# Performance work log

Hardware: AMD Instinct MI355X
Metric: run time of the kernel (lower is better)

The kernel has to match this reference:

```python
import jax, jax.numpy as jnp
import numpy as np

NFFT = 512
HOP = 256
N_FREQ = NFFT // 2


def _imdct_kernels():
    # Matches _get_imdct_kernels: windowed IMDCT cosine basis, shape [nfft, nfft//2]
    def kernel_fn(time, freq):
        win = np.sin(np.pi * (2 * time + 1) / (2.0 * NFFT))
        return np.cos(np.pi / NFFT * (2 * time + 1 + NFFT / 2.0) * (freq + 0.5)) * win
    k = np.fromfunction(kernel_fn, (NFFT, N_FREQ), dtype=np.float64)
    return jnp.asarray(k.astype(np.float32))  # [nfft, n_freq]


def setup_inputs() -> dict:
    key = jax.random.key(0)
    spec = jax.random.normal(key, (16, 1, N_FREQ, 4096), dtype=jnp.float32)
    return {"spec": spec, "kernels": _imdct_kernels()}


def reference(spec, kernels):
    # spec: [B, 1, n_freq, T]; kernels: [nfft, n_freq]
    B, _, _, T = spec.shape
    # conv2d with (n_freq,1) kernel == per-frame basis matmul over frequency
    frames = jnp.einsum('bft,kf->btk', spec[:, 0], kernels) * (4.0 / NFFT)  # [B, T, nfft]
    # conv_transpose2d with identity-diagonal kernel and stride=hop == overlap-add
    L = (T - 1) * HOP + NFFT
    idx = jnp.arange(T)[:, None] * HOP + jnp.arange(NFFT)[None, :]  # [T, nfft]
    out = jnp.zeros((B, L), dtype=spec.dtype).at[:, idx].add(frames)
    return out
```

## Files before the change

kernel.cpp:

```cpp
#include <hip/hip_runtime.h>
#include <stdint.h>

#define NFREQ 256
#define NB 16
#define NT 4096
#define LOUT 1048832
#define TROWS 65
#define TROW 132

typedef __bf16 bf16;
typedef __bf16 bf16x8 __attribute__((ext_vector_type(8)));
typedef float floatx4 __attribute__((ext_vector_type(4)));

__device__ inline uint32_t f_as_u(float x) { union { float f; uint32_t u; } v; v.f = x; return v.u; }
__device__ inline uint32_t bf16r(float x) {
    uint32_t u = f_as_u(x);
    return (u + 0x7fffu + ((u >> 16) & 1u)) >> 16;
}

__global__ __launch_bounds__(256) void build_kb(const float* __restrict__ ker,
                                                bf16* __restrict__ kbF) {
    int idx = blockIdx.x * 256 + threadIdx.x;
    int n = idx >> 9, f = idx & 511;
    float v = (f < 256) ? ker[(n + 256) * 256 + f] : ker[n * 256 + (f - 256)];
    uint32_t rr = bf16r(v * 0.0078125f);
    union { uint16_t u; bf16 b; } o; o.u = (uint16_t)rr;
    kbF[((size_t)(f >> 5) * 256 + n) * 32 + (f & 31)] = o.b;
}

__global__ __launch_bounds__(256, 4) void imdct_gemm(const float* __restrict__ spec,
                                                     const bf16* __restrict__ kbF,
                                                     float* __restrict__ out) {
    __shared__ uint32_t Tt[TROWS * TROW];

    const int jt = blockIdx.x;
    const int b  = blockIdx.y;
    const int tid = threadIdx.x, lane = tid & 63, w = tid >> 6;
    const int j0 = jt * 64;
    const float* sb = spec + (size_t)b * NFREQ * NT;

    {
        const int lpar = lane & 1, lt = lane >> 1;
        const int fpw = w * 32;
        for (int rb = 0; rb < 4; ++rb) {
            float v[16];
            #pragma unroll
            for (int i = 0; i < 16; ++i) {
                int r = rb * 16 + i;
                int tc = r >> 5, fpi = r & 31;
                int f = (fpw + fpi) * 2 + lpar;
                int t = j0 - 1 + tc * 32 + lt;
                v[i] = ((unsigned)t < (unsigned)NT) ? sb[(size_t)f * NT + t] : 0.0f;
            }
            #pragma unroll
            for (int i = 0; i < 16; i += 2) {
                int r = rb * 16 + i;
                int tc = r >> 5, fpi = r & 31;
                int tl = tc * 32 + lt;
                uint32_t h0 = bf16r(v[i]);     uint32_t o0 = (uint32_t)__shfl_xor((int)h0, 1);
                uint32_t h1 = bf16r(v[i + 1]); uint32_t o1 = (uint32_t)__shfl_xor((int)h1, 1);
                if (lpar == 0) {
                    uint2 pk; pk.x = (h0 & 0xffffu) | (o0 << 16); pk.y = (h1 & 0xffffu) | (o1 << 16);
                    *reinterpret_cast<uint2*>(&Tt[tl * TROW + fpw + fpi]) = pk;
                }
            }
        }
        int f = w * 64 + lane;
        int t = j0 + 63;
        float v = ((unsigned)t < (unsigned)NT) ? sb[(size_t)f * NT + t] : 0.0f;
        uint32_t h = bf16r(v); uint32_t o = (uint32_t)__shfl_xor((int)h, 1);
        if (lpar == 0) Tt[64 * TROW + w * 32 + lt] = (h & 0xffffu) | (o << 16);
    }
    __syncthreads();

    const int row16 = lane & 15, q = lane >> 4;
    floatx4 acc[4][4] = {};
    const uint8_t* Tb = reinterpret_cast<const uint8_t*>(Tt);
    const bf16* kbw = kbF + (size_t)w * 64 * 32;

    for (int kki = 0; kki < 8; ++kki) {
        const int toff = (kki >= 4) ? 1 : 0;
        const int kbyte = (kki & 3) * 128;
        #pragma unroll
        for (int ks = 0; ks < 2; ++ks) {
            const int kchunk = kki * 2 + ks;
            bf16x8 af[4], bfr[4];
            #pragma unroll
            for (int i = 0; i < 4; ++i)
                af[i] = *reinterpret_cast<const bf16x8*>(
                    Tb + (size_t)(i * 16 + row16 + toff) * 528 + kbyte + ks * 64 + q * 16);
            #pragma unroll
            for (int jn = 0; jn < 4; ++jn)
                bfr[jn] = *reinterpret_cast<const bf16x8*>(
                    kbw + (size_t)kchunk * 8192 + (jn * 16 + row16) * 32 + q * 8);
            #pragma unroll
            for (int i = 0; i < 4; ++i)
                #pragma unroll
                for (int jn = 0; jn < 4; ++jn)
                    acc[i][jn] = __builtin_amdgcn_mfma_f32_16x16x32_bf16(af[i], bfr[jn], acc[i][jn], 0, 0, 0);
        }
    }

    #pragma unroll
    for (int i = 0; i < 4; ++i) {
        #pragma unroll
        for (int e = 0; e < 4; ++e) {
            int j = j0 + i * 16 + q * 4 + e;
            if (j <= 4096) {
                float* orow = out + (size_t)b * LOUT + (size_t)j * 256 + w * 64;
                #pragma unroll
                for (int jn = 0; jn < 4; ++jn)
                    orow[jn * 16 + row16] = acc[i][jn][e];
            }
        }
    }
}

extern "C" void kernel_launch(void* const* d_in, const int* in_sizes, int n_in,
                              void* d_out, int out_size, void* d_ws, size_t ws_size,
                              hipStream_t stream) {
    const float* spec = (const float*)d_in[0];
    const float* ker  = (const float*)d_in[1];
    float* out = (float*)d_out;

    bf16* kbF = (bf16*)d_ws;

    build_kb<<<512, 256, 0, stream>>>(ker, kbF);
    imdct_gemm<<<dim3(65, NB), 256, 0, stream>>>(spec, kbF, out);
}
```

Baseline: 142.8 us.

## Double time tile per block and vectorize spectrum staging loads

Each block now covers 128 output hop-rows instead of 64, so every weight fragment loaded from global memory is reused across 8 M-tiles instead of 4, and the grid shrinks from 65 to 33 column tiles. The spectrum staging is rewritten to use float4 loads along time with a different shuffle/pack scheme, and bf16 rounding switches from round-to-nearest-even to simple round-half-up. The cost is twice the accumulator registers and LDS per block, with occupancy hints lowered to 2, and a grid of 33x16 blocks that may underfill the GPU.

```diff
diff --git a/kernel.cpp b/kernel.cpp
--- a/kernel.cpp
+++ b/kernel.cpp
@@ -5,104 +5,96 @@
 #define NB 16
 #define NT 4096
 #define LOUT 1048832
-#define TROWS 65
-#define TROW 132
+#define TROWS 129
+#define TROWSZ 132
 
 typedef __bf16 bf16;
 typedef __bf16 bf16x8 __attribute__((ext_vector_type(8)));
 typedef float floatx4 __attribute__((ext_vector_type(4)));
 
 __device__ inline uint32_t f_as_u(float x) { union { float f; uint32_t u; } v; v.f = x; return v.u; }
-__device__ inline uint32_t bf16r(float x) {
-    uint32_t u = f_as_u(x);
-    return (u + 0x7fffu + ((u >> 16) & 1u)) >> 16;
-}
 
 __global__ __launch_bounds__(256) void build_kb(const float* __restrict__ ker,
                                                 bf16* __restrict__ kbF) {
     int idx = blockIdx.x * 256 + threadIdx.x;
     int n = idx >> 9, f = idx & 511;
     float v = (f < 256) ? ker[(n + 256) * 256 + f] : ker[n * 256 + (f - 256)];
-    uint32_t rr = bf16r(v * 0.0078125f);
+    uint32_t u = f_as_u(v * 0.0078125f);
+    uint32_t rr = (u + 0x7fffu + ((u >> 16) & 1u)) >> 16;
     union { uint16_t u; bf16 b; } o; o.u = (uint16_t)rr;
     kbF[((size_t)(f >> 5) * 256 + n) * 32 + (f & 31)] = o.b;
 }
 
-__global__ __launch_bounds__(256, 4) void imdct_gemm(const float* __restrict__ spec,
+__global__ __launch_bounds__(256, 2) void imdct_gemm(const float* __restrict__ spec,
                                                      const bf16* __restrict__ kbF,
                                                      float* __restrict__ out) {
-    __shared__ uint32_t Tt[TROWS * TROW];
+    __shared__ uint32_t Tt[TROWS * TROWSZ];
 
     const int jt = blockIdx.x;
     const int b  = blockIdx.y;
     const int tid = threadIdx.x, lane = tid & 63, w = tid >> 6;
-    const int j0 = jt * 64;
+    const int j0 = jt * 128;
     const float* sb = spec + (size_t)b * NFREQ * NT;
 
     {
-        const int lpar = lane & 1, lt = lane >> 1;
-        const int fpw = w * 32;
-        for (int rb = 0; rb < 4; ++rb) {
-            float v[16];
+        const int fr = lane >> 2;
+        const int par = fr & 1;
+        const int tsub = lane & 3;
+        for (int u = 0; u < 9; ++u) {
+            int tc = tsub + u * 4;
+            bool tcok = (tc <= 32);
             #pragma unroll
-            for (int i = 0; i < 16; ++i) {
-                int r = rb * 16 + i;
-                int tc = r >> 5, fpi = r & 31;
-                int f = (fpw + fpi) * 2 + lpar;
-                int t = j0 - 1 + tc * 32 + lt;
-                v[i] = ((unsigned)t < (unsigned)NT) ? sb[(size_t)f * NT + t] : 0.0f;
-            }
-            #pragma unroll
-            for (int i = 0; i < 16; i += 2) {
-                int r = rb * 16 + i;
-                int tc = r >> 5, fpi = r & 31;
-                int tl = tc * 32 + lt;
-                uint32_t h0 = bf16r(v[i]);     uint32_t o0 = (uint32_t)__shfl_xor((int)h0, 1);
-                uint32_t h1 = bf16r(v[i + 1]); uint32_t o1 = (uint32_t)__shfl_xor((int)h1, 1);
-                if (lpar == 0) {
-                    uint2 pk; pk.x = (h0 & 0xffffu) | (o0 << 16); pk.y = (h1 & 0xffffu) | (o1 << 16);
-                    *reinterpret_cast<uint2*>(&Tt[tl * TROW + fpw + fpi]) = pk;
+            for (int fo = 0; fo < 64; fo += 16) {
+                int f = w * 64 + fo + fr;
+                int t0 = j0 - 4 + tc * 4;
+                floatx4 v = {0.f, 0.f, 0.f, 0.f};
+                if (tcok && t0 >= 0 && t0 <= NT - 4)
+                    v = *reinterpret_cast<const floatx4*>(sb + (size_t)f * NT + t0);
+                uint32_t h[4], o[4];
+                #pragma unroll
+                for (int e = 0; e < 4; ++e) h[e] = (f_as_u(v[e]) + 0x8000u) >> 16;
+                #pragma unroll
+                for (int e = 0; e < 4; ++e) o[e] = (uint32_t)__shfl_xor((int)h[e], 4);
+                uint32_t pk0 = par ? ((o[2] & 0xffffu) | (h[2] << 16))
+                                   : ((h[0] & 0xffffu) | (o[0] << 16));
+                uint32_t pk1 = par ? ((o[3] & 0xffffu) | (h[3] << 16))
+                                   : ((h[1] & 0xffffu) | (o[1] << 16));
+                int fp = (w * 64 + fo) / 2 + (fr >> 1);
+                int tw0 = tc * 4 - 3 + par * 2;
+                if (tcok) {
+                    if ((unsigned)tw0 <= 128u)       Tt[tw0 * TROWSZ + fp]       = pk0;
+                    if ((unsigned)(tw0 + 1) <= 128u) Tt[(tw0 + 1) * TROWSZ + fp] = pk1;
                 }
             }
         }
-        int f = w * 64 + lane;
-        int t = j0 + 63;
-        float v = ((unsigned)t < (unsigned)NT) ? sb[(size_t)f * NT + t] : 0.0f;
-        uint32_t h = bf16r(v); uint32_t o = (uint32_t)__shfl_xor((int)h, 1);
-        if (lpar == 0) Tt[64 * TROW + w * 32 + lt] = (h & 0xffffu) | (o << 16);
     }
     __syncthreads();
 
     const int row16 = lane & 15, q = lane >> 4;
-    floatx4 acc[4][4] = {};
+    floatx4 acc[8][4] = {};
     const uint8_t* Tb = reinterpret_cast<const uint8_t*>(Tt);
     const bf16* kbw = kbF + (size_t)w * 64 * 32;
 
-    for (int kki = 0; kki < 8; ++kki) {
-        const int toff = (kki >= 4) ? 1 : 0;
-        const int kbyte = (kki & 3) * 128;
+    #pragma unroll 2
+    for (int kki = 0; kki < 16; ++kki) {
+        bf16x8 bfr[4];
         #pragma unroll
-        for (int ks = 0; ks < 2; ++ks) {
-            const int kchunk = kki * 2 + ks;
-            bf16x8 af[4], bfr[4];
-            #pragma unroll
-            for (int i = 0; i < 4; ++i)
-                af[i] = *reinterpret_cast<const bf16x8*>(
-                    Tb + (size_t)(i * 16 + row16 + toff) * 528 + kbyte + ks * 64 + q * 16);
+        for (int jn = 0; jn < 4; ++jn)
+            bfr[jn] = *reinterpret_cast<const bf16x8*>(
+                kbw + (size_t)kki * 8192 + (jn * 16 + row16) * 32 + q * 8);
+        const uint8_t* Ta = Tb + (size_t)(row16 + (kki >= 8 ? 1 : 0)) * 528
+                               + (kki & 7) * 64 + q * 16;
+        #pragma unroll
+        for (int i = 0; i < 8; ++i) {
+            bf16x8 af = *reinterpret_cast<const bf16x8*>(Ta + (size_t)i * 16 * 528);
             #pragma unroll
             for (int jn = 0; jn < 4; ++jn)
-                bfr[jn] = *reinterpret_cast<const bf16x8*>(
-                    kbw + (size_t)kchunk * 8192 + (jn * 16 + row16) * 32 + q * 8);
-            #pragma unroll
-            for (int i = 0; i < 4; ++i)
-                #pragma unroll
-                for (int jn = 0; jn < 4; ++jn)
-                    acc[i][jn] = __builtin_amdgcn_mfma_f32_16x16x32_bf16(af[i], bfr[jn], acc[i][jn], 0, 0, 0);
+                acc[i][jn] = __builtin_amdgcn_mfma_f32_16x16x32_bf16(af, bfr[jn], acc[i][jn], 0, 0, 0);
         }
     }
 
     #pragma unroll
-    for (int i = 0; i < 4; ++i) {
+    for (int i = 0; i < 8; ++i) {
         #pragma unroll
         for (int e = 0; e < 4; ++e) {
             int j = j0 + i * 16 + q * 4 + e;
@@ -126,5 +118,5 @@
     bf16* kbF = (bf16*)d_ws;
 
     build_kb<<<512, 256, 0, stream>>>(ker, kbF);
-    imdct_gemm<<<dim3(65, NB), 256, 0, stream>>>(spec, kbF, out);
+    imdct_gemm<<<dim3(33, NB), 256, 0, stream>>>(spec, kbF, out);
 }
```

After: 146.7 us. 2.8% more time.
